# Kernel tuning notes

Measured on AMD Instinct MI355X. Metric: run time of the kernel, lower is better.

## Reference

```python
import jax, jax.numpy as jnp
import numpy as np

B, L, C, H = 2, 512, 256, 8
D = C // H
LN_EPS = 1e-5


def setup_inputs() -> dict:
    key = jax.random.key(0)
    ks = jax.random.split(key, 9)
    s = lambda fan: 1.0 / np.sqrt(fan)
    return {
        "x": jax.random.normal(ks[0], (B, L, C), dtype=jnp.float32),
        "relative_pos": jax.random.normal(ks[1], (B, L, L, C), dtype=jnp.float32),
        "w_qkv": jax.random.normal(ks[2], (3 * C, C), dtype=jnp.float32) * s(C),
        "w_rel": jax.random.normal(ks[3], (H, C), dtype=jnp.float32) * s(C),
        "b_rel": jax.random.normal(ks[4], (H,), dtype=jnp.float32) * 0.02,
        "ln_gamma": jnp.ones((H,), dtype=jnp.float32),
        "ln_beta": jnp.zeros((H,), dtype=jnp.float32),
        "w_proj": jax.random.normal(ks[5], (C, C), dtype=jnp.float32) * s(C),
        "b_proj": jnp.zeros((C,), dtype=jnp.float32),
    }


def reference(x, relative_pos, w_qkv, w_rel, b_rel, ln_gamma, ln_beta, w_proj, b_proj):
    scale = D ** -0.5
    # qkv projection: [B,L,3C] -> [3,B,H,L,D]
    qkv = (x @ w_qkv.T).reshape(B, L, 3, H, D).transpose(2, 0, 3, 1, 4)
    q, k, v = qkv[0], qkv[1], qkv[2]
    # relative bias: Linear -> exact GELU -> LayerNorm over head dim
    rel = relative_pos @ w_rel.T + b_rel          # [B,L,L,H]
    rel = jax.nn.gelu(rel, approximate=False)
    mu = jnp.mean(rel, axis=-1, keepdims=True)
    var = jnp.mean(jnp.square(rel - mu), axis=-1, keepdims=True)
    rel = (rel - mu) * jax.lax.rsqrt(var + LN_EPS) * ln_gamma + ln_beta
    rel = rel.transpose(0, 3, 1, 2)               # [B,H,L,L]
    # attention (bias added pre-scale, matching the original)
    attn = (jnp.einsum("bhld,bhmd->bhlm", q, k) + rel) * scale
    attn = jax.nn.softmax(attn, axis=-1)
    out = jnp.einsum("bhlm,bhmd->bhld", attn, v)  # [B,H,L,D]
    out = out.transpose(0, 2, 1, 3).reshape(B, L, C)
    return out @ w_proj.T + b_proj
```

## Files before the change

kernel.cpp:

```cpp
#include <hip/hip_runtime.h>
#include <hip/hip_bf16.h>
#include <math.h>

#define BB 2
#define LL 512
#define CC 256
#define HH 8
#define DD 32
#define LN_EPS 1e-5f
#define SCALE 0.17677669529663687f
#define RSQRT2 0.70710678118654752f

__global__ __launch_bounds__(256) void k1_qkv(const float* __restrict__ x,
                                              const float* __restrict__ w,
                                              float* __restrict__ qkv_out) {
    __shared__ float xs[16][64];
    __shared__ float wsd[16][64];
    const int row0 = blockIdx.x * 64;
    const int col0 = blockIdx.y * 64;
    const int t  = threadIdx.x;
    const int ry = t >> 4;
    const int cx = t & 15;
    const int lr = t >> 2;
    const int lq = t & 3;
    float acc[4][4] = {};
    for (int k0 = 0; k0 < 256; k0 += 16) {
        float4 xv = *(const float4*)(x + (row0 + lr) * 256 + k0 + 4 * lq);
        float4 wv = *(const float4*)(w + (col0 + lr) * 256 + k0 + 4 * lq);
        xs[4*lq+0][lr] = xv.x; xs[4*lq+1][lr] = xv.y;
        xs[4*lq+2][lr] = xv.z; xs[4*lq+3][lr] = xv.w;
        wsd[4*lq+0][lr] = wv.x; wsd[4*lq+1][lr] = wv.y;
        wsd[4*lq+2][lr] = wv.z; wsd[4*lq+3][lr] = wv.w;
        __syncthreads();
#pragma unroll
        for (int kk = 0; kk < 16; ++kk) {
            float4 a  = *(const float4*)&xs[kk][4*ry];
            float4 bb = *(const float4*)&wsd[kk][4*cx];
            float av[4] = {a.x, a.y, a.z, a.w};
            float bv[4] = {bb.x, bb.y, bb.z, bb.w};
#pragma unroll
            for (int rr = 0; rr < 4; ++rr)
#pragma unroll
                for (int cc = 0; cc < 4; ++cc)
                    acc[rr][cc] = fmaf(av[rr], bv[cc], acc[rr][cc]);
        }
        __syncthreads();
    }
#pragma unroll
    for (int rr = 0; rr < 4; ++rr) {
        const int row = row0 + 4*ry + rr;
        const int b = row >> 9, l = row & 511;
#pragma unroll
        for (int cc = 0; cc < 4; ++cc) {
            const int o = col0 + 4*cx + cc;
            const int three = o >> 8;
            const int hh = (o >> 5) & 7;
            const int dd = o & 31;
            qkv_out[three * 262144 + ((b*8 + hh)*512 + l)*32 + dd] = acc[rr][cc];
        }
    }
}

__global__ __launch_bounds__(256) void k2_rel(const float* __restrict__ rp,
                                              const float* __restrict__ wr,
                                              const float* __restrict__ br,
                                              const float* __restrict__ gam_p,
                                              const float* __restrict__ bet_p,
                                              float* __restrict__ rel_t) {
    __shared__ float rps[32 * 260];
    __shared__ float wls[8 * 260];
    __shared__ float st[8][33];
    const int t   = threadIdx.x;
    const int blk = blockIdx.x;
    const int jt  = blk & 15;
    const int i   = (blk >> 4) & 511;
    const int b   = blk >> 13;
    const int j0  = jt << 5;

    {
        const float4* ws4 = (const float4*)wr;
        int idx = t;
        int hh = idx >> 6, c4 = idx & 63;
        *(float4*)&wls[hh * 260 + 4 * c4] = ws4[idx];
        idx = t + 256;
        hh = idx >> 6; c4 = idx & 63;
        *(float4*)&wls[hh * 260 + 4 * c4] = ws4[idx];
    }
    const int jr = t >> 3;
    const int u  = t & 7;
    const float4* rsrc = (const float4*)(rp + (((long)(b * 512 + i) * 512) + j0 + jr) * 256);
#pragma unroll
    for (int c = 0; c < 8; ++c)
        *(float4*)&rps[jr * 260 + 4 * (u + 8 * c)] = rsrc[u + 8 * c];
    __syncthreads();

    const int h = t & 7;
    const float* ar   = &rps[jr * 260];
    const float* wrow = &wls[h * 260];
    float4 acc = {0.f, 0.f, 0.f, 0.f};
#pragma unroll 8
    for (int c4 = 0; c4 < 64; ++c4) {
        float4 a = *(const float4*)&ar[4 * c4];
        float4 w = *(const float4*)&wrow[4 * c4];
        acc.x = fmaf(a.x, w.x, acc.x);
        acc.y = fmaf(a.y, w.y, acc.y);
        acc.z = fmaf(a.z, w.z, acc.z);
        acc.w = fmaf(a.w, w.w, acc.w);
    }
    float r = ((acc.x + acc.y) + (acc.z + acc.w)) + br[h];
    float g = 0.5f * r * (1.0f + erff(r * RSQRT2));
    float sg = g, sg2 = g * g;
    sg += __shfl_xor(sg, 1); sg2 += __shfl_xor(sg2, 1);
    sg += __shfl_xor(sg, 2); sg2 += __shfl_xor(sg2, 2);
    sg += __shfl_xor(sg, 4); sg2 += __shfl_xor(sg2, 4);
    const float mu  = sg * 0.125f;
    const float var = fmaf(sg2, 0.125f, -mu * mu);
    const float o = fmaf((g - mu) * rsqrtf(var + LN_EPS), gam_p[h], bet_p[h]);
    st[h][jr] = o;
    __syncthreads();
    const int h2 = t >> 5, j2 = t & 31;
    rel_t[(((long)(b * 8 + h2) * 512) + i) * 512 + j0 + j2] = st[h2][j2];
}

__global__ __launch_bounds__(256) void k3_attn(const float* __restrict__ qg,
                                               const float* __restrict__ kg,
                                               const float* __restrict__ vg,
                                               const float* __restrict__ rel_t,
                                               float* __restrict__ outg) {
    __shared__ float p_lds[4][512];
    const int lane = threadIdx.x & 63;
    const int wid  = threadIdx.x >> 6;
    const int row  = blockIdx.x * 4 + wid;
    const int b = row >> 12;
    const int h = (row >> 9) & 7;
    const int i = row & 511;

    const float* qp = qg + ((b*8 + h)*512 + i) * 32;
    float4 qv[8];
#pragma unroll
    for (int dd = 0; dd < 8; ++dd)
        qv[dd] = *(const float4*)(qp + 4 * dd);

    const float* kp0  = kg + (long)((b*8 + h)*512) * 32;
    const float* relp = rel_t + (((long)(b*8 + h)*512) + i) * 512;

    float sc[8];
#pragma unroll
    for (int tt = 0; tt < 8; ++tt) {
        const int j = lane + 64 * tt;
        const float* kp = kp0 + j * 32;
        float acc = 0.0f;
#pragma unroll
        for (int dd = 0; dd < 8; ++dd) {
            float4 k4 = *(const float4*)(kp + 4 * dd);
            acc = fmaf(qv[dd].x, k4.x, acc);
            acc = fmaf(qv[dd].y, k4.y, acc);
            acc = fmaf(qv[dd].z, k4.z, acc);
            acc = fmaf(qv[dd].w, k4.w, acc);
        }
        sc[tt] = (acc + relp[j]) * SCALE;
    }
    float m = sc[0];
#pragma unroll
    for (int tt = 1; tt < 8; ++tt) m = fmaxf(m, sc[tt]);
    m = fmaxf(m, __shfl_xor(m, 1));
    m = fmaxf(m, __shfl_xor(m, 2));
    m = fmaxf(m, __shfl_xor(m, 4));
    m = fmaxf(m, __shfl_xor(m, 8));
    m = fmaxf(m, __shfl_xor(m, 16));
    m = fmaxf(m, __shfl_xor(m, 32));
    float sum = 0.0f;
#pragma unroll
    for (int tt = 0; tt < 8; ++tt) { sc[tt] = __expf(sc[tt] - m); sum += sc[tt]; }
    sum += __shfl_xor(sum, 1);
    sum += __shfl_xor(sum, 2);
    sum += __shfl_xor(sum, 4);
    sum += __shfl_xor(sum, 8);
    sum += __shfl_xor(sum, 16);
    sum += __shfl_xor(sum, 32);
    const float inv = 1.0f / sum;
#pragma unroll
    for (int tt = 0; tt < 8; ++tt)
        p_lds[wid][lane + 64 * tt] = sc[tt] * inv;
    __syncthreads();

    const int d = lane & 31;
    const int half = lane >> 5;
    const float* vp = vg + (long)((b*8 + h)*512) * 32 + (half * 256) * 32 + d;
    const float* pw = &p_lds[wid][half * 256];
    float a0 = 0.f, a1 = 0.f, a2 = 0.f, a3 = 0.f;
#pragma unroll 4
    for (int jj = 0; jj < 256; jj += 4) {
        a0 = fmaf(pw[jj + 0], vp[(jj + 0) * 32], a0);
        a1 = fmaf(pw[jj + 1], vp[(jj + 1) * 32], a1);
        a2 = fmaf(pw[jj + 2], vp[(jj + 2) * 32], a2);
        a3 = fmaf(pw[jj + 3], vp[(jj + 3) * 32], a3);
    }
    float acc = (a0 + a1) + (a2 + a3);
    acc += __shfl_xor(acc, 32);
    if (lane < 32)
        outg[(b*512 + i) * 256 + h * 32 + d] = acc;
}

__global__ __launch_bounds__(256) void k4_proj(const float* __restrict__ a_in,
                                               const float* __restrict__ w,
                                               const float* __restrict__ bp,
                                               float* __restrict__ outg) {
    __shared__ float xs[16][64];
    __shared__ float wsd[16][64];
    const int row0 = blockIdx.x * 64;
    const int col0 = blockIdx.y * 64;
    const int t  = threadIdx.x;
    const int ry = t >> 4;
    const int cx = t & 15;
    const int lr = t >> 2;
    const int lq = t & 3;
    float acc[4][4] = {};
    for (int k0 = 0; k0 < 256; k0 += 16) {
        float4 xv = *(const float4*)(a_in + (row0 + lr) * 256 + k0 + 4 * lq);
        float4 wv = *(const float4*)(w + (col0 + lr) * 256 + k0 + 4 * lq);
        xs[4*lq+0][lr] = xv.x; xs[4*lq+1][lr] = xv.y;
        xs[4*lq+2][lr] = xv.z; xs[4*lq+3][lr] = xv.w;
        wsd[4*lq+0][lr] = wv.x; wsd[4*lq+1][lr] = wv.y;
        wsd[4*lq+2][lr] = wv.z; wsd[4*lq+3][lr] = wv.w;
        __syncthreads();
#pragma unroll
        for (int kk = 0; kk < 16; ++kk) {
            float4 a  = *(const float4*)&xs[kk][4*ry];
            float4 bb = *(const float4*)&wsd[kk][4*cx];
            float av[4] = {a.x, a.y, a.z, a.w};
            float bv[4] = {bb.x, bb.y, bb.z, bb.w};
#pragma unroll
            for (int rr = 0; rr < 4; ++rr)
#pragma unroll
                for (int cc = 0; cc < 4; ++cc)
                    acc[rr][cc] = fmaf(av[rr], bv[cc], acc[rr][cc]);
        }
        __syncthreads();
    }
#pragma unroll
    for (int rr = 0; rr < 4; ++rr) {
        const int row = row0 + 4*ry + rr;
#pragma unroll
        for (int cc = 0; cc < 4; ++cc) {
            const int col = col0 + 4*cx + cc;
            outg[row * 256 + col] = acc[rr][cc] + bp[col];
        }
    }
}

extern "C" void kernel_launch(void* const* d_in, const int* in_sizes, int n_in,
                              void* d_out, int out_size, void* d_ws, size_t ws_size,
                              hipStream_t stream) {
    const float* x      = (const float*)d_in[0];
    const float* rp     = (const float*)d_in[1];
    const float* w_qkv  = (const float*)d_in[2];
    const float* w_rel  = (const float*)d_in[3];
    const float* b_rel  = (const float*)d_in[4];
    const float* gamma  = (const float*)d_in[5];
    const float* beta   = (const float*)d_in[6];
    const float* w_proj = (const float*)d_in[7];
    const float* b_proj = (const float*)d_in[8];
    float* out = (float*)d_out;
    float* ws  = (float*)d_ws;

    float* q     = ws;
    float* kk    = ws + 262144;
    float* vv    = ws + 524288;
    float* rel_t = ws + 786432;
    float* attn  = ws + 786432 + 4194304;

    k1_qkv<<<dim3(16, 12), 256, 0, stream>>>(x, w_qkv, q);
    k2_rel<<<16384, 256, 0, stream>>>(rp, w_rel, b_rel, gamma, beta, rel_t);
    k3_attn<<<2048, 256, 0, stream>>>(q, kk, vv, rel_t, attn);
    k4_proj<<<dim3(16, 4), 256, 0, stream>>>(attn, w_proj, b_proj, out);
}
```

Measured before the change: 830.8 us.

## Register-resident rel-bias projection, transposed K layout for coalesced score computation

The rel-bias kernel no longer stages the 256-channel rows in shared memory. Each lane keeps an 8-channel slice of w_rel in registers, streams rows with a one-step register prefetch, and reduces across lanes with shuffles, so each block now covers 64 columns instead of 32. The QKV kernel writes K transposed ([bh][d][l]), which lets the attention kernel read K and the rel bias as coalesced float4 vectors, with each lane computing 8 contiguous scores and writing P as float4. The cost is more shuffle traffic and register pressure in exchange for removing LDS staging and strided K reads.

```diff
diff --git a/kernel.cpp b/kernel.cpp
--- a/kernel.cpp
+++ b/kernel.cpp
@@ -56,7 +56,12 @@
             const int three = o >> 8;
             const int hh = (o >> 5) & 7;
             const int dd = o & 31;
-            qkv_out[three * 262144 + ((b*8 + hh)*512 + l)*32 + dd] = acc[rr][cc];
+            int idx;
+            if (three == 1)
+                idx = 262144 + ((b*8 + hh)*32 + dd)*512 + l;
+            else
+                idx = three * 262144 + ((b*8 + hh)*512 + l)*32 + dd;
+            qkv_out[idx] = acc[rr][cc];
         }
     }
 }
@@ -67,63 +72,96 @@
                                               const float* __restrict__ gam_p,
                                               const float* __restrict__ bet_p,
                                               float* __restrict__ rel_t) {
-    __shared__ float rps[32 * 260];
-    __shared__ float wls[8 * 260];
-    __shared__ float st[8][33];
-    const int t   = threadIdx.x;
-    const int blk = blockIdx.x;
-    const int jt  = blk & 15;
-    const int i   = (blk >> 4) & 511;
-    const int b   = blk >> 13;
-    const int j0  = jt << 5;
-
+    __shared__ float st[8][65];
+    const int t    = threadIdx.x;
+    const int lane = t & 63;
+    const int wid  = t >> 6;
+    const int blk  = blockIdx.x;
+    const int jt = blk & 7;
+    const int i  = (blk >> 3) & 511;
+    const int b  = blk >> 12;
+    const int j0 = jt << 6;
+    const int chunk = lane & 31;
+    const int jh    = lane >> 5;
+    const int h     = lane & 7;
+
+    float wreg[8][8];
     {
-        const float4* ws4 = (const float4*)wr;
-        int idx = t;
-        int hh = idx >> 6, c4 = idx & 63;
-        *(float4*)&wls[hh * 260 + 4 * c4] = ws4[idx];
-        idx = t + 256;
-        hh = idx >> 6; c4 = idx & 63;
-        *(float4*)&wls[hh * 260 + 4 * c4] = ws4[idx];
-    }
-    const int jr = t >> 3;
-    const int u  = t & 7;
-    const float4* rsrc = (const float4*)(rp + (((long)(b * 512 + i) * 512) + j0 + jr) * 256);
-#pragma unroll
-    for (int c = 0; c < 8; ++c)
-        *(float4*)&rps[jr * 260 + 4 * (u + 8 * c)] = rsrc[u + 8 * c];
-    __syncthreads();
-
-    const int h = t & 7;
-    const float* ar   = &rps[jr * 260];
-    const float* wrow = &wls[h * 260];
-    float4 acc = {0.f, 0.f, 0.f, 0.f};
-#pragma unroll 8
-    for (int c4 = 0; c4 < 64; ++c4) {
-        float4 a = *(const float4*)&ar[4 * c4];
-        float4 w = *(const float4*)&wrow[4 * c4];
-        acc.x = fmaf(a.x, w.x, acc.x);
-        acc.y = fmaf(a.y, w.y, acc.y);
-        acc.z = fmaf(a.z, w.z, acc.z);
-        acc.w = fmaf(a.w, w.w, acc.w);
-    }
-    float r = ((acc.x + acc.y) + (acc.z + acc.w)) + br[h];
-    float g = 0.5f * r * (1.0f + erff(r * RSQRT2));
-    float sg = g, sg2 = g * g;
-    sg += __shfl_xor(sg, 1); sg2 += __shfl_xor(sg2, 1);
-    sg += __shfl_xor(sg, 2); sg2 += __shfl_xor(sg2, 2);
-    sg += __shfl_xor(sg, 4); sg2 += __shfl_xor(sg2, 4);
-    const float mu  = sg * 0.125f;
-    const float var = fmaf(sg2, 0.125f, -mu * mu);
-    const float o = fmaf((g - mu) * rsqrtf(var + LN_EPS), gam_p[h], bet_p[h]);
-    st[h][jr] = o;
+        const float4* wr4 = (const float4*)wr;
+#pragma unroll
+        for (int hh = 0; hh < 8; ++hh) {
+            float4 w0 = wr4[hh*64 + chunk*2];
+            float4 w1 = wr4[hh*64 + chunk*2 + 1];
+            wreg[hh][0]=w0.x; wreg[hh][1]=w0.y; wreg[hh][2]=w0.z; wreg[hh][3]=w0.w;
+            wreg[hh][4]=w1.x; wreg[hh][5]=w1.y; wreg[hh][6]=w1.z; wreg[hh][7]=w1.w;
+        }
+    }
+    const float brv = br[h], gmv = gam_p[h], btv = bet_p[h];
+
+    const float* base = rp + ((long)(b*512 + i)*512 + (j0 + wid*16 + jh)) * 256
+                           + chunk*8;
+    float4 a0 = *(const float4*)(base);
+    float4 a1 = *(const float4*)(base + 4);
+#pragma unroll
+    for (int it = 0; it < 8; ++it) {
+        float4 n0 = a0, n1 = a1;
+        if (it < 7) {
+            const float* np = base + (2*(it+1))*256;
+            n0 = *(const float4*)(np);
+            n1 = *(const float4*)(np + 4);
+        }
+        float acc[8];
+#pragma unroll
+        for (int hh = 0; hh < 8; ++hh) {
+            float s = 0.f;
+            s = fmaf(a0.x, wreg[hh][0], s);
+            s = fmaf(a0.y, wreg[hh][1], s);
+            s = fmaf(a0.z, wreg[hh][2], s);
+            s = fmaf(a0.w, wreg[hh][3], s);
+            s = fmaf(a1.x, wreg[hh][4], s);
+            s = fmaf(a1.y, wreg[hh][5], s);
+            s = fmaf(a1.z, wreg[hh][6], s);
+            s = fmaf(a1.w, wreg[hh][7], s);
+            acc[hh] = s;
+        }
+#pragma unroll
+        for (int hh = 0; hh < 8; ++hh) acc[hh] += __shfl_xor(acc[hh], 1);
+#pragma unroll
+        for (int hh = 0; hh < 8; ++hh) acc[hh] += __shfl_xor(acc[hh], 2);
+#pragma unroll
+        for (int hh = 0; hh < 8; ++hh) acc[hh] += __shfl_xor(acc[hh], 4);
+        float v0 = (h & 1) ? acc[1] : acc[0];
+        float v1 = (h & 1) ? acc[3] : acc[2];
+        float v2 = (h & 1) ? acc[5] : acc[4];
+        float v3 = (h & 1) ? acc[7] : acc[6];
+        float u0 = (h & 2) ? v1 : v0;
+        float u1 = (h & 2) ? v3 : v2;
+        float tot = (h & 4) ? u1 : u0;
+        tot += __shfl_xor(tot, 8);
+        tot += __shfl_xor(tot, 16);
+
+        const float r = tot + brv;
+        const float g = 0.5f * r * (1.0f + erff(r * RSQRT2));
+        float sg = g, sg2 = g * g;
+        sg += __shfl_xor(sg, 1); sg2 += __shfl_xor(sg2, 1);
+        sg += __shfl_xor(sg, 2); sg2 += __shfl_xor(sg2, 2);
+        sg += __shfl_xor(sg, 4); sg2 += __shfl_xor(sg2, 4);
+        const float mu  = sg * 0.125f;
+        const float var = fmaf(sg2, 0.125f, -mu * mu);
+        const float o = fmaf((g - mu) * rsqrtf(var + LN_EPS), gmv, btv);
+        if ((lane & 31) < 8)
+            st[h][wid*16 + 2*it + jh] = o;
+        a0 = n0; a1 = n1;
+    }
     __syncthreads();
     const int h2 = t >> 5, j2 = t & 31;
-    rel_t[(((long)(b * 8 + h2) * 512) + i) * 512 + j0 + j2] = st[h2][j2];
+    const long orow = ((long)(b*8 + h2) * 512 + i) * 512 + j0;
+    rel_t[orow + j2]      = st[h2][j2];
+    rel_t[orow + j2 + 32] = st[h2][j2 + 32];
 }
 
 __global__ __launch_bounds__(256) void k3_attn(const float* __restrict__ qg,
-                                               const float* __restrict__ kg,
+                                               const float* __restrict__ kt,
                                                const float* __restrict__ vg,
                                                const float* __restrict__ rel_t,
                                                float* __restrict__ outg) {
@@ -134,44 +172,47 @@
     const int b = row >> 12;
     const int h = (row >> 9) & 7;
     const int i = row & 511;
-
-    const float* qp = qg + ((b*8 + h)*512 + i) * 32;
-    float4 qv[8];
-#pragma unroll
-    for (int dd = 0; dd < 8; ++dd)
-        qv[dd] = *(const float4*)(qp + 4 * dd);
-
-    const float* kp0  = kg + (long)((b*8 + h)*512) * 32;
-    const float* relp = rel_t + (((long)(b*8 + h)*512) + i) * 512;
-
-    float sc[8];
-#pragma unroll
-    for (int tt = 0; tt < 8; ++tt) {
-        const int j = lane + 64 * tt;
-        const float* kp = kp0 + j * 32;
-        float acc = 0.0f;
-#pragma unroll
-        for (int dd = 0; dd < 8; ++dd) {
-            float4 k4 = *(const float4*)(kp + 4 * dd);
-            acc = fmaf(qv[dd].x, k4.x, acc);
-            acc = fmaf(qv[dd].y, k4.y, acc);
-            acc = fmaf(qv[dd].z, k4.z, acc);
-            acc = fmaf(qv[dd].w, k4.w, acc);
-        }
-        sc[tt] = (acc + relp[j]) * SCALE;
-    }
-    float m = sc[0];
-#pragma unroll
-    for (int tt = 1; tt < 8; ++tt) m = fmaxf(m, sc[tt]);
+    const int bh = b*8 + h;
+
+    const float* qp = qg + (bh*512 + i) * 32;
+    float qs[32];
+#pragma unroll
+    for (int dd = 0; dd < 8; ++dd) {
+        float4 q4 = *(const float4*)(qp + 4*dd);
+        qs[4*dd+0]=q4.x; qs[4*dd+1]=q4.y; qs[4*dd+2]=q4.z; qs[4*dd+3]=q4.w;
+    }
+    const float4* kt4  = (const float4*)(kt + (long)bh * 32 * 512);
+    const float4* rel4 = (const float4*)(rel_t + ((long)bh * 512 + i) * 512);
+
+    float4 s0 = {0.f,0.f,0.f,0.f}, s1 = {0.f,0.f,0.f,0.f};
+#pragma unroll
+    for (int dd = 0; dd < 32; ++dd) {
+        float4 ka = kt4[dd*128 + lane];
+        float4 kb = kt4[dd*128 + 64 + lane];
+        const float qd = qs[dd];
+        s0.x = fmaf(qd, ka.x, s0.x); s0.y = fmaf(qd, ka.y, s0.y);
+        s0.z = fmaf(qd, ka.z, s0.z); s0.w = fmaf(qd, ka.w, s0.w);
+        s1.x = fmaf(qd, kb.x, s1.x); s1.y = fmaf(qd, kb.y, s1.y);
+        s1.z = fmaf(qd, kb.z, s1.z); s1.w = fmaf(qd, kb.w, s1.w);
+    }
+    float4 r0 = rel4[lane], r1 = rel4[64 + lane];
+    s0.x = (s0.x + r0.x) * SCALE; s0.y = (s0.y + r0.y) * SCALE;
+    s0.z = (s0.z + r0.z) * SCALE; s0.w = (s0.w + r0.w) * SCALE;
+    s1.x = (s1.x + r1.x) * SCALE; s1.y = (s1.y + r1.y) * SCALE;
+    s1.z = (s1.z + r1.z) * SCALE; s1.w = (s1.w + r1.w) * SCALE;
+    float m = fmaxf(fmaxf(fmaxf(s0.x, s0.y), fmaxf(s0.z, s0.w)),
+                    fmaxf(fmaxf(s1.x, s1.y), fmaxf(s1.z, s1.w)));
     m = fmaxf(m, __shfl_xor(m, 1));
     m = fmaxf(m, __shfl_xor(m, 2));
     m = fmaxf(m, __shfl_xor(m, 4));
     m = fmaxf(m, __shfl_xor(m, 8));
     m = fmaxf(m, __shfl_xor(m, 16));
     m = fmaxf(m, __shfl_xor(m, 32));
-    float sum = 0.0f;
-#pragma unroll
-    for (int tt = 0; tt < 8; ++tt) { sc[tt] = __expf(sc[tt] - m); sum += sc[tt]; }
+    s0.x = __expf(s0.x - m); s0.y = __expf(s0.y - m);
+    s0.z = __expf(s0.z - m); s0.w = __expf(s0.w - m);
+    s1.x = __expf(s1.x - m); s1.y = __expf(s1.y - m);
+    s1.z = __expf(s1.z - m); s1.w = __expf(s1.w - m);
+    float sum = ((s0.x + s0.y) + (s0.z + s0.w)) + ((s1.x + s1.y) + (s1.z + s1.w));
     sum += __shfl_xor(sum, 1);
     sum += __shfl_xor(sum, 2);
     sum += __shfl_xor(sum, 4);
@@ -179,14 +220,15 @@
     sum += __shfl_xor(sum, 16);
     sum += __shfl_xor(sum, 32);
     const float inv = 1.0f / sum;
-#pragma unroll
-    for (int tt = 0; tt < 8; ++tt)
-        p_lds[wid][lane + 64 * tt] = sc[tt] * inv;
+    s0.x *= inv; s0.y *= inv; s0.z *= inv; s0.w *= inv;
+    s1.x *= inv; s1.y *= inv; s1.z *= inv; s1.w *= inv;
+    *(float4*)&p_lds[wid][4*lane]       = s0;
+    *(float4*)&p_lds[wid][256 + 4*lane] = s1;
     __syncthreads();
 
     const int d = lane & 31;
     const int half = lane >> 5;
-    const float* vp = vg + (long)((b*8 + h)*512) * 32 + (half * 256) * 32 + d;
+    const float* vp = vg + (long)(bh*512) * 32 + (half * 256) * 32 + d;
     const float* pw = &p_lds[wid][half * 256];
     float a0 = 0.f, a1 = 0.f, a2 = 0.f, a3 = 0.f;
 #pragma unroll 4
@@ -271,7 +313,7 @@
     float* attn  = ws + 786432 + 4194304;
 
     k1_qkv<<<dim3(16, 12), 256, 0, stream>>>(x, w_qkv, q);
-    k2_rel<<<16384, 256, 0, stream>>>(rp, w_rel, b_rel, gamma, beta, rel_t);
+    k2_rel<<<8192, 256, 0, stream>>>(rp, w_rel, b_rel, gamma, beta, rel_t);
     k3_attn<<<2048, 256, 0, stream>>>(q, kk, vv, rel_t, attn);
     k4_proj<<<dim3(16, 4), 256, 0, stream>>>(attn, w_proj, b_proj, out);
 }
```

Result: faster. 766.0 us (-7.8%).
